# Kernel tuning notes

Measured on AMD Instinct MI355X. Metric: run time of the kernel, lower is better.

## Reference

```python
import jax, jax.numpy as jnp
import numpy as np

N, T, D_FEAT, H = 8192, 60, 6, 64
NEG_SLOPE = 0.01  # torch LeakyReLU default


def setup_inputs() -> dict:
    key = jax.random.key(0)
    ks = jax.random.split(key, 20)
    s = lambda k, shape, fan: jax.random.normal(k, shape, jnp.float32) * (1.0 / np.sqrt(fan))
    inp = {
        'x': jax.random.normal(ks[0], (N, T, D_FEAT), jnp.float32),
        # LSTM layer 0 (input D_FEAT) and layer 1 (input H); gate order i,f,g,o
        'Wih0': s(ks[1], (4 * H, D_FEAT), H), 'Whh0': s(ks[2], (4 * H, H), H),
        'bih0': s(ks[3], (4 * H,), H), 'bhh0': s(ks[4], (4 * H,), H),
        'Wih1': s(ks[5], (4 * H, H), H), 'Whh1': s(ks[6], (4 * H, H), H),
        'bih1': s(ks[7], (4 * H,), H), 'bhh1': s(ks[8], (4 * H,), H),
        # GAT layer: transformation Linear(H,H) and attention vector a [2H,1] (randn in torch)
        'Wt': s(ks[9], (H, H), H), 'bt': s(ks[10], (H,), H),
        'a': jax.random.normal(ks[11], (2 * H, 1), jnp.float32),
        # fc and fc_out
        'Wfc': s(ks[12], (H, H), H), 'bfc': s(ks[13], (H,), H),
        'Wout': s(ks[14], (1, H), H), 'bout': s(ks[15], (1,), H),
    }
    return inp


def _lstm_layer(x, Wih, Whh, bih, bhh):
    # x: [N, T, Din] -> outputs [N, T, H]
    xg = jnp.einsum('ntd,gd->ntg', x, Wih) + bih + bhh  # precompute input gates

    def step(carry, xt):
        h, c = carry
        gates = xt + h @ Whh.T  # [N, 4H]
        i, f, g, o = jnp.split(gates, 4, axis=-1)
        c = jax.nn.sigmoid(f) * c + jax.nn.sigmoid(i) * jnp.tanh(g)
        h = jax.nn.sigmoid(o) * jnp.tanh(c)
        return (h, c), h

    n = x.shape[0]
    h0 = jnp.zeros((n, Whh.shape[1]), x.dtype)
    (_, _), hs = jax.lax.scan(step, (h0, h0), jnp.swapaxes(xg, 0, 1))
    return jnp.swapaxes(hs, 0, 1)


def _gat_layer(x, Wt, bt, a):
    # att[i,j] = leaky_relu(a1 . Wx_j + a2 . Wx_i); softmax over j; out = att @ x
    h = x @ Wt.T + bt                    # [N, H]
    hdim = h.shape[1]
    s1 = (h @ a[:hdim]).squeeze(-1)      # a1 . Wx_j  -> column term
    s2 = (h @ a[hdim:]).squeeze(-1)      # a2 . Wx_i  -> row term
    scores = jax.nn.leaky_relu(s2[:, None] + s1[None, :], NEG_SLOPE)  # [N, N]
    att = jax.nn.softmax(scores, axis=1)
    return att @ x


def reference(x, Wih0, Whh0, bih0, bhh0, Wih1, Whh1, bih1, bhh1,
              Wt, bt, a, Wfc, bfc, Wout, bout):
    out = _lstm_layer(x, Wih0, Whh0, bih0, bhh0)
    out = _lstm_layer(out, Wih1, Whh1, bih1, bhh1)
    last = out[:, -1, :]                 # [N, H]
    hidden = _gat_layer(last, Wt, bt, a) + last  # num_layers_gat = 1
    hidden = jax.nn.leaky_relu(hidden @ Wfc.T + bfc, NEG_SLOPE)
    return (hidden @ Wout.T + bout).squeeze(-1)  # [N]
```

## Files before the change

### kernel.cpp

```cpp
#include <hip/hip_runtime.h>

#define NN 8192
#define TT 60
#define DF 6
#define HH 64
#define GG 256
#define RS 132
#define CH 32
#define NB 256

typedef _Float16 half8 __attribute__((ext_vector_type(8)));
typedef float f32x4 __attribute__((ext_vector_type(4)));
#define MFMA16(a, b, c) __builtin_amdgcn_mfma_f32_16x16x32_f16((a), (b), (c), 0, 0, 0)

#define LOG2E 1.44269504f

__device__ __forceinline__ float lrelu_(float x) { return x > 0.0f ? x : 0.01f * x; }

__device__ __forceinline__ float lstm_act2(float gi, float gf, float gg, float go,
                                           float& c)
{
    const float ei = __builtin_amdgcn_exp2f(gi * -LOG2E);
    const float ef = __builtin_amdgcn_exp2f(gf * -LOG2E);
    const float eg = __builtin_amdgcn_exp2f(fminf(gg * (-2.f * LOG2E), 63.f));
    const float sf = __builtin_amdgcn_rcpf(1.f + ef);
    const float tg_si = (1.f - eg) * __builtin_amdgcn_rcpf((1.f + ei) * (1.f + eg));
    c = __builtin_fmaf(sf, c, tg_si);
    const float eo = __builtin_amdgcn_exp2f(go * -LOG2E);
    const float ec = __builtin_amdgcn_exp2f(fminf(c * (-2.f * LOG2E), 63.f));
    return (1.f - ec) * __builtin_amdgcn_rcpf((1.f + eo) * (1.f + ec));
}

__device__ __forceinline__ half8 ldw8(const float* __restrict__ p) {
    const float4* q = (const float4*)p;
    float4 u = q[0], v = q[1];
    half8 r;
    r[0]=(_Float16)u.x; r[1]=(_Float16)u.y; r[2]=(_Float16)u.z; r[3]=(_Float16)u.w;
    r[4]=(_Float16)v.x; r[5]=(_Float16)v.y; r[6]=(_Float16)v.z; r[7]=(_Float16)v.w;
    return r;
}

#define SXW (TT * 8 + 8)

__global__ __launch_bounds__(512, 4)
void lstm_fused_kernel(const float* __restrict__ x,
                       const float* __restrict__ Wih0, const float* __restrict__ Whh0,
                       const float* __restrict__ bih0, const float* __restrict__ bhh0,
                       const float* __restrict__ Wih1, const float* __restrict__ Whh1,
                       const float* __restrict__ bih1, const float* __restrict__ bhh1,
                       const float* __restrict__ Wt, const float* __restrict__ bt,
                       const float* __restrict__ av,
                       float* __restrict__ last_out,
                       float* __restrict__ s1g, float* __restrict__ s2g)
{
    __shared__ _Float16 sxp[16][SXW];
    __shared__ _Float16 h0buf[2][16][72];
    __shared__ _Float16 h1buf[2][16][72];
    __shared__ _Float16 zero16[8];
    __shared__ float sv1[HH], sv2[HH], sc12[2];

    const int tid  = threadIdx.x;
    const int w    = tid >> 6;
    const int grp  = w >> 2;
    const int cg   = w & 3;
    const int lane = tid & 63;
    const int quad = lane >> 4;
    const int l15  = lane & 15;
    const int hc   = cg * 16 + l15;
    const int n0   = blockIdx.x * 16;

    for (int i = tid; i < 16 * SXW / 2; i += 512) ((unsigned*)sxp)[i] = 0u;
    for (int i = tid; i < 2 * 16 * 72 / 2; i += 512) ((unsigned*)h0buf)[i] = 0u;
    for (int i = tid; i < 2 * 16 * 72 / 2; i += 512) ((unsigned*)h1buf)[i] = 0u;
    if (tid < 4) ((unsigned*)zero16)[tid] = 0u;
    __syncthreads();

    for (int idx = tid; idx < 16 * TT * DF; idx += 512) {
        const int m = idx / (TT * DF);
        const int r = idx - m * (TT * DF);
        const int t = r / DF;
        const int d = r - t * DF;
        sxp[m][t * 8 + d] = (_Float16)x[(size_t)(n0 + m) * (TT * DF) + r];
    }

    if (tid < HH) {
        float a1 = 0.f, a2 = 0.f;
        #pragma unroll 8
        for (int h = 0; h < HH; h++) {
            const float wt = Wt[h * HH + tid];
            a1 += wt * av[h];
            a2 += wt * av[HH + h];
        }
        sv1[tid] = a1; sv2[tid] = a2;
    } else if (tid == 64 || tid == 65) {
        const float* ap = av + (tid - 64) * HH;
        float c = 0.f;
        #pragma unroll 8
        for (int h = 0; h < HH; h++) c += bt[h] * ap[h];
        sc12[tid - 64] = c;
    }

    half8 wA[4][2], wB[4][2];
    float bias[4];
    half8 hzero;
    #pragma unroll
    for (int j = 0; j < 8; j++) hzero[j] = (_Float16)0.f;

    if (grp == 0) {
        #pragma unroll
        for (int nt = 0; nt < 4; nt++) {
            const int g = nt * 64 + hc;
            wA[nt][0] = ldw8(Whh0 + (size_t)g * HH + quad * 8);
            wA[nt][1] = ldw8(Whh0 + (size_t)g * HH + 32 + quad * 8);
            bias[nt]  = bih0[g] + bhh0[g];
            half8 t = hzero;
            if (quad == 0) {
                #pragma unroll
                for (int j = 0; j < DF; j++) t[j] = (_Float16)Wih0[g * DF + j];
            }
            wB[nt][0] = t;
            wB[nt][1] = hzero;
        }
    } else {
        #pragma unroll
        for (int nt = 0; nt < 4; nt++) {
            const int g = nt * 64 + hc;
            wA[nt][0] = ldw8(Wih1 + (size_t)g * HH + quad * 8);
            wA[nt][1] = ldw8(Wih1 + (size_t)g * HH + 32 + quad * 8);
            wB[nt][0] = ldw8(Whh1 + (size_t)g * HH + quad * 8);
            wB[nt][1] = ldw8(Whh1 + (size_t)g * HH + 32 + quad * 8);
            bias[nt]  = bih1[g] + bhh1[g];
        }
    }

    float cs[4] = {0.f, 0.f, 0.f, 0.f};
    __syncthreads();

    for (int i = 0; i <= TT; i++) {
        const int p = i & 1;
        if (grp == 0) {
            if (i < TT) {
                const half8 a0 = *(const half8*)&h0buf[p][l15][quad * 8];
                const half8 a1 = *(const half8*)&h0buf[p][l15][32 + quad * 8];
                const _Float16* xap = (quad == 0) ? &sxp[l15][i * 8] : zero16;
                const half8 ax = *(const half8*)xap;
                f32x4 gv[4];
                #pragma unroll
                for (int nt = 0; nt < 4; nt++) {
                    f32x4 c; c[0] = bias[nt]; c[1] = bias[nt]; c[2] = bias[nt]; c[3] = bias[nt];
                    c = MFMA16(ax, wB[nt][0], c);
                    c = MFMA16(a0, wA[nt][0], c);
                    c = MFMA16(a1, wA[nt][1], c);
                    gv[nt] = c;
                }
                _Float16 (*h0w)[72] = h0buf[p ^ 1];
                #pragma unroll
                for (int reg = 0; reg < 4; reg++) {
                    const float hv = lstm_act2(gv[0][reg], gv[1][reg], gv[2][reg], gv[3][reg], cs[reg]);
                    h0w[quad * 4 + reg][hc] = (_Float16)hv;
                }
            }
        } else {
            if (i > 0) {
                const half8 a00 = *(const half8*)&h0buf[p][l15][quad * 8];
                const half8 a01 = *(const half8*)&h0buf[p][l15][32 + quad * 8];
                const half8 a10 = *(const half8*)&h1buf[p][l15][quad * 8];
                const half8 a11 = *(const half8*)&h1buf[p][l15][32 + quad * 8];
                f32x4 gv[4];
                #pragma unroll
                for (int nt = 0; nt < 4; nt++) {
                    f32x4 c; c[0] = bias[nt]; c[1] = bias[nt]; c[2] = bias[nt]; c[3] = bias[nt];
                    c = MFMA16(a00, wA[nt][0], c);
                    c = MFMA16(a01, wA[nt][1], c);
                    c = MFMA16(a10, wB[nt][0], c);
                    c = MFMA16(a11, wB[nt][1], c);
                    gv[nt] = c;
                }
                _Float16 (*h1w)[72] = h1buf[p ^ 1];
                #pragma unroll
                for (int reg = 0; reg < 4; reg++) {
                    const float hv = lstm_act2(gv[0][reg], gv[1][reg], gv[2][reg], gv[3][reg], cs[reg]);
                    h1w[quad * 4 + reg][hc] = (_Float16)hv;
                    if (i == TT) last_out[(size_t)(n0 + quad * 4 + reg) * HH + hc] = hv;
                }
            }
        }
        __syncthreads();
    }

    {
        const _Float16 (*hf)[72] = h1buf[1];
        const int r  = tid >> 5;
        const int c0 = tid & 31;
        const float h1a = (float)hf[r][c0];
        const float h1b = (float)hf[r][c0 + 32];
        float p1 = h1a * sv1[c0] + h1b * sv1[c0 + 32];
        float p2 = h1a * sv2[c0] + h1b * sv2[c0 + 32];
        #pragma unroll
        for (int off = 16; off > 0; off >>= 1) {
            p1 += __shfl_xor(p1, off);
            p2 += __shfl_xor(p2, off);
        }
        if (c0 == 0) {
            s1g[n0 + r] = p1 + sc12[0];
            s2g[n0 + r] = p2 + sc12[1];
        }
    }
}

__global__ __launch_bounds__(1024)
void rankfac_kernel(const float* __restrict__ s1g, const float* __restrict__ s2g,
                    float* __restrict__ Z, float* __restrict__ Ai, float* __restrict__ Bi,
                    float* __restrict__ U, float* __restrict__ W,
                    int* __restrict__ iperm, float* __restrict__ sortedD)
{
    __shared__ float sb[NN];
    __shared__ float sredw[16];
    __shared__ int   sRank[32];
    const int tid  = threadIdx.x;
    const int lane = tid & 63;
    const int wv   = tid >> 6;
    const int b    = blockIdx.x;
    const int j0   = b * 32;

    for (int idx = tid; idx < NN; idx += 1024) sb[idx] = s1g[idx];
    if (tid < 32) sRank[tid] = 0;
    __syncthreads();

    float m = -1e30f;
    for (int idx = tid; idx < NN; idx += 1024) m = fmaxf(m, sb[idx]);
    #pragma unroll
    for (int off = 32; off > 0; off >>= 1) m = fmaxf(m, __shfl_xor(m, off));
    if (lane == 0) sredw[wv] = m;
    __syncthreads();
    if (tid == 0) {
        float mm = sredw[0];
        #pragma unroll
        for (int q = 1; q < 16; q++) mm = fmaxf(mm, sredw[q]);
        sredw[0] = mm;
    }
    __syncthreads();
    const float s1max = sredw[0];

    if (tid < 32) {
        const int j = j0 + tid;
        const float z  = s2g[j] + s1max;
        const float mi = lrelu_(z);
        Z[j]  = z;
        Ai[j] = __expf(z - mi);
        Bi[j] = __expf(0.01f * z - mi);
        const float d = sb[j] - s1max;
        U[j] = __expf(d);
        W[j] = __expf(0.01f * d);
    }
    {
        const int jl = tid & 31;
        const int part = tid >> 5;
        const float sj = sb[j0 + jl];
        const int jg = j0 + jl;
        const int k0 = part * (NN / 32);
        const float4* sb4 = (const float4*)&sb[k0];
        int cnt = 0;
        #pragma unroll 8
        for (int it = 0; it < NN / 32 / 4; it++) {
            const float4 v = sb4[it];
            const int kb = k0 + it * 4;
            cnt += (v.x < sj || (v.x == sj && kb + 0 < jg)) ? 1 : 0;
            cnt += (v.y < sj || (v.y == sj && kb + 1 < jg)) ? 1 : 0;
            cnt += (v.z < sj || (v.z == sj && kb + 2 < jg)) ? 1 : 0;
            cnt += (v.w < sj || (v.w == sj && kb + 3 < jg)) ? 1 : 0;
        }
        atomicAdd(&sRank[jl], cnt);
    }
    __syncthreads();
    if (tid < 32) {
        const int r = sRank[tid];
        iperm[r] = j0 + tid;
        sortedD[r] = sb[j0 + tid] - s1max;
    }
}

__global__ __launch_bounds__(256)
void scanA_kernel(const float* __restrict__ last, const float* __restrict__ U,
                  const float* __restrict__ W, const int* __restrict__ iperm,
                  float* __restrict__ chunkSum)
{
    __shared__ int   sj[CH];
    __shared__ float su[CH], sw[CH];
    __shared__ float al[CH][HH], bl[CH][HH];
    const int tid = threadIdx.x;
    const int b   = blockIdx.x;
    if (tid < CH) {
        const int j = iperm[b * CH + tid];
        sj[tid] = j; su[tid] = U[j]; sw[tid] = W[j];
    }
    __syncthreads();
    for (int idx = tid; idx < CH * HH; idx += 256) {
        const int rr = idx >> 6, c = idx & 63;
        const float lv = last[(size_t)sj[rr] * HH + c];
        al[rr][c] = su[rr] * lv;
        bl[rr][c] = sw[rr] * lv;
    }
    __syncthreads();
    if (tid < 130) {
        const int c = tid;
        float s = 0.f;
        if (c < 64) {
            for (int rr = 0; rr < CH; rr++) s += al[rr][c];
        } else if (c < 128) {
            for (int rr = 0; rr < CH; rr++) s += bl[rr][c - 64];
        } else if (c == 128) {
            for (int rr = 0; rr < CH; rr++) s += su[rr];
        } else {
            for (int rr = 0; rr < CH; rr++) s += sw[rr];
        }
        chunkSum[b * RS + c] = s;
    }
}

__global__ __launch_bounds__(256)
void scanC_kernel(const float* __restrict__ last, const float* __restrict__ U,
                  const float* __restrict__ W, const int* __restrict__ iperm,
                  const float* __restrict__ chunkSum, float* __restrict__ PP)
{
    __shared__ int   sj[CH];
    __shared__ float su[CH], sw[CH];
    __shared__ float al[CH][HH], bl[CH][HH];
    const int tid = threadIdx.x;
    const int b   = blockIdx.x;
    if (tid < CH) {
        const int j = iperm[b * CH + tid];
        sj[tid] = j; su[tid] = U[j]; sw[tid] = W[j];
    }
    __syncthreads();
    for (int idx = tid; idx < CH * HH; idx += 256) {
        const int rr = idx >> 6, c = idx & 63;
        const float lv = last[(size_t)sj[rr] * HH + c];
        al[rr][c] = su[rr] * lv;
        bl[rr][c] = sw[rr] * lv;
    }
    __syncthreads();
    if (tid < 130) {
        const int c = tid;
        const bool rev = (c < 64) || (c == 128);
        float run = 0.f;
        if (rev) {
            #pragma unroll 8
            for (int k = 0; k < NB; k++)
                run += (k > b) ? chunkSum[k * RS + c] : 0.f;
            if (b == NB - 1) PP[(size_t)NN * RS + c] = 0.f;
            for (int rr = CH - 1; rr >= 0; rr--) {
                const float val = (c < 64) ? al[rr][c] : su[rr];
                run += val;
                PP[(size_t)(b * CH + rr) * RS + c] = run;
            }
        } else {
            #pragma unroll 8
            for (int k = 0; k < NB; k++)
                run += (k < b) ? chunkSum[k * RS + c] : 0.f;
            for (int rr = 0; rr < CH; rr++) {
                PP[(size_t)(b * CH + rr) * RS + c] = run;
                run += (c < 128) ? bl[rr][c - 64] : sw[rr];
            }
            if (b == NB - 1) PP[(size_t)NN * RS + c] = run;
        }
    }
}

__global__ __launch_bounds__(512)
void applyfc_kernel(const float* __restrict__ last,
                    const float* __restrict__ Z, const float* __restrict__ Ai, const float* __restrict__ Bi,
                    const float* __restrict__ sortedD, const float* __restrict__ PP,
                    const float* __restrict__ Wfc, const float* __restrict__ bfc,
                    const float* __restrict__ Wout, const float* __restrict__ bout,
                    float* __restrict__ out)
{
    __shared__ float sdD[NN];
    __shared__ float sW[HH][HH + 1];
    __shared__ float sbF[HH], saF[HH];
    const int tid = threadIdx.x;
    for (int idx = tid; idx < NN; idx += 512) sdD[idx] = sortedD[idx];
    for (int idx = tid; idx < HH * HH; idx += 512) {
        const int h = idx >> 6, d = idx & 63;
        sW[d][h] = Wfc[idx];
    }
    if (tid < HH) { sbF[tid] = bfc[tid]; saF[tid] = Wout[tid]; }
    __syncthreads();

    const int wv = tid >> 6, lane = tid & 63;
    const int i0 = blockIdx.x * 32 + wv * 4;
    float zi[4]; int lo[4], hi[4];
    #pragma unroll
    for (int q = 0; q < 4; q++) { zi[q] = Z[i0 + q]; lo[q] = 0; hi[q] = NN; }
    for (int iter = 0; iter < 13; iter++) {
        #pragma unroll
        for (int q = 0; q < 4; q++) {
            if (lo[q] < hi[q]) {
                const int mid = (lo[q] + hi[q]) >> 1;
                const float dm = sdD[mid];
                if (zi[q] + dm > 0.f) hi[q] = mid; else lo[q] = mid + 1;
            }
        }
    }
    float gv[4];
    #pragma unroll
    for (int q = 0; q < 4; q++) {
        const int i = i0 + q;
        const float* rowp = PP + (size_t)lo[q] * RS;
        const float pu  = rowp[lane];
        const float pw  = rowp[64 + lane];
        const float pud = rowp[128];
        const float pwd = rowp[129];
        const float ai = Ai[i], bi = Bi[i];
        const float numer = bi * pw + ai * pu;
        const float den   = bi * pwd + ai * pud;
        const float lv = last[(size_t)i * HH + lane];
        gv[q] = numer * __builtin_amdgcn_rcpf(den) + lv;
    }
    const float bo = bout[0];
    #pragma unroll
    for (int q = 0; q < 4; q++) {
        float acc = sbF[lane];
        #pragma unroll
        for (int d = 0; d < HH; d++) acc += __shfl(gv[q], d) * sW[d][lane];
        float prod = lrelu_(acc) * saF[lane];
        #pragma unroll
        for (int off = 32; off > 0; off >>= 1) prod += __shfl_xor(prod, off);
        if (lane == 0) out[i0 + q] = prod + bo;
    }
}

extern "C" void kernel_launch(void* const* d_in, const int* in_sizes, int n_in,
                              void* d_out, int out_size, void* d_ws, size_t ws_size,
                              hipStream_t stream)
{
    (void)in_sizes; (void)n_in; (void)out_size; (void)ws_size;
    const float* x    = (const float*)d_in[0];
    const float* Wih0 = (const float*)d_in[1];
    const float* Whh0 = (const float*)d_in[2];
    const float* bih0 = (const float*)d_in[3];
    const float* bhh0 = (const float*)d_in[4];
    const float* Wih1 = (const float*)d_in[5];
    const float* Whh1 = (const float*)d_in[6];
    const float* bih1 = (const float*)d_in[7];
    const float* bhh1 = (const float*)d_in[8];
    const float* Wt   = (const float*)d_in[9];
    const float* bt   = (const float*)d_in[10];
    const float* a    = (const float*)d_in[11];
    const float* Wfc  = (const float*)d_in[12];
    const float* bfc  = (const float*)d_in[13];
    const float* Wout = (const float*)d_in[14];
    const float* bout = (const float*)d_in[15];
    float* out = (float*)d_out;

    float* ws       = (float*)d_ws;
    float* last     = ws;
    float* s1g      = last + (size_t)NN*HH;
    float* s2g      = s1g + NN;
    float* Z        = s2g + NN;
    float* Ai       = Z + NN;
    float* Bi       = Ai + NN;
    float* U        = Bi + NN;
    float* W        = U + NN;
    float* sortedD  = W + NN;
    int*   iperm    = (int*)(sortedD + NN);
    float* chunkSum = (float*)(iperm + NN);
    float* chunkOfs = chunkSum + NB*RS;
    float* PP       = chunkOfs + NB*RS;

    lstm_fused_kernel<<<dim3(NN / 16), dim3(512), 0, stream>>>(
        x, Wih0, Whh0, bih0, bhh0, Wih1, Whh1, bih1, bhh1,
        Wt, bt, a, last, s1g, s2g);
    rankfac_kernel<<<dim3(NB), dim3(1024), 0, stream>>>(
        s1g, s2g, Z, Ai, Bi, U, W, iperm, sortedD);
    scanA_kernel<<<dim3(NB), dim3(256), 0, stream>>>(last, U, W, iperm, chunkSum);
    scanC_kernel<<<dim3(NB), dim3(256), 0, stream>>>(last, U, W, iperm, chunkSum, PP);
    applyfc_kernel<<<dim3(NB), dim3(512), 0, stream>>>(
        last, Z, Ai, Bi, sortedD, PP, Wfc, bfc, Wout, bout, out);
}
```

Before: 243.5 us.

## Merge post-LSTM kernels into one persistent kernel with grid barriers

Fuses the rank/factor, two scan passes and the apply/fc stage into a single 256-block kernel that uses atomic-counter grid barriers in place of kernel launch boundaries. The barrier counters are reset by the LSTM kernel. The shared al/bl tiles are reused between the two scan phases, so the second gather of last is gone. This is meant to remove three launch gaps and one redundant gather. In exchange it depends on all 256 1024-thread blocks being co-resident (deadlock risk otherwise), leaves the apply stage with half the rows per wave, and uses a spin-wait barrier.

```diff
diff --git a/kernel.cpp b/kernel.cpp
--- a/kernel.cpp
+++ b/kernel.cpp
@@ -40,6 +40,18 @@
     return r;
 }
 
+__device__ __forceinline__ void gridbar(int* cnt, int tid)
+{
+    __syncthreads();
+    if (tid == 0) {
+        __threadfence();
+        __hip_atomic_fetch_add(cnt, 1, __ATOMIC_ACQ_REL, __HIP_MEMORY_SCOPE_AGENT);
+        while (__hip_atomic_load(cnt, __ATOMIC_RELAXED, __HIP_MEMORY_SCOPE_AGENT) < NB) {}
+        __threadfence();
+    }
+    __syncthreads();
+}
+
 #define SXW (TT * 8 + 8)
 
 __global__ __launch_bounds__(512, 4)
@@ -51,7 +63,8 @@
                        const float* __restrict__ Wt, const float* __restrict__ bt,
                        const float* __restrict__ av,
                        float* __restrict__ last_out,
-                       float* __restrict__ s1g, float* __restrict__ s2g)
+                       float* __restrict__ s1g, float* __restrict__ s2g,
+                       int* __restrict__ barp)
 {
     __shared__ _Float16 sxp[16][SXW];
     __shared__ _Float16 h0buf[2][16][72];
@@ -68,6 +81,8 @@
     const int l15  = lane & 15;
     const int hc   = cg * 16 + l15;
     const int n0   = blockIdx.x * 16;
+
+    if (blockIdx.x == 0 && tid < 3) barp[tid] = 0;
 
     for (int i = tid; i < 16 * SXW / 2; i += 512) ((unsigned*)sxp)[i] = 0u;
     for (int i = tid; i < 2 * 16 * 72 / 2; i += 512) ((unsigned*)h0buf)[i] = 0u;
@@ -209,14 +224,25 @@
 }
 
 __global__ __launch_bounds__(1024)
-void rankfac_kernel(const float* __restrict__ s1g, const float* __restrict__ s2g,
-                    float* __restrict__ Z, float* __restrict__ Ai, float* __restrict__ Bi,
-                    float* __restrict__ U, float* __restrict__ W,
-                    int* __restrict__ iperm, float* __restrict__ sortedD)
+void post_kernel(const float* __restrict__ last,
+                 const float* __restrict__ s1g, const float* __restrict__ s2g,
+                 float* __restrict__ Z, float* __restrict__ Ai, float* __restrict__ Bi,
+                 float* __restrict__ U, float* __restrict__ W,
+                 int* __restrict__ iperm, float* __restrict__ sortedD,
+                 float* __restrict__ chunkSum, float* __restrict__ PP,
+                 const float* __restrict__ Wfc, const float* __restrict__ bfc,
+                 const float* __restrict__ Wout, const float* __restrict__ bout,
+                 float* __restrict__ out, int* __restrict__ barp)
 {
     __shared__ float sb[NN];
     __shared__ float sredw[16];
     __shared__ int   sRank[32];
+    __shared__ int   sj[CH];
+    __shared__ float su[CH], sw[CH];
+    __shared__ float al[CH][HH], bl[CH][HH];
+    __shared__ float sW[HH][HH + 1];
+    __shared__ float sbF[HH], saF[HH];
+
     const int tid  = threadIdx.x;
     const int lane = tid & 63;
     const int wv   = tid >> 6;
@@ -256,7 +282,7 @@
     {
         const int jl = tid & 31;
         const int part = tid >> 5;
-        const float sj = sb[j0 + jl];
+        const float sjv = sb[j0 + jl];
         const int jg = j0 + jl;
         const int k0 = part * (NN / 32);
         const float4* sb4 = (const float4*)&sb[k0];
@@ -265,10 +291,10 @@
         for (int it = 0; it < NN / 32 / 4; it++) {
             const float4 v = sb4[it];
             const int kb = k0 + it * 4;
-            cnt += (v.x < sj || (v.x == sj && kb + 0 < jg)) ? 1 : 0;
-            cnt += (v.y < sj || (v.y == sj && kb + 1 < jg)) ? 1 : 0;
-            cnt += (v.z < sj || (v.z == sj && kb + 2 < jg)) ? 1 : 0;
-            cnt += (v.w < sj || (v.w == sj && kb + 3 < jg)) ? 1 : 0;
+            cnt += (v.x < sjv || (v.x == sjv && kb + 0 < jg)) ? 1 : 0;
+            cnt += (v.y < sjv || (v.y == sjv && kb + 1 < jg)) ? 1 : 0;
+            cnt += (v.z < sjv || (v.z == sjv && kb + 2 < jg)) ? 1 : 0;
+            cnt += (v.w < sjv || (v.w == sjv && kb + 3 < jg)) ? 1 : 0;
         }
         atomicAdd(&sRank[jl], cnt);
     }
@@ -278,24 +304,15 @@
         iperm[r] = j0 + tid;
         sortedD[r] = sb[j0 + tid] - s1max;
     }
-}
-
-__global__ __launch_bounds__(256)
-void scanA_kernel(const float* __restrict__ last, const float* __restrict__ U,
-                  const float* __restrict__ W, const int* __restrict__ iperm,
-                  float* __restrict__ chunkSum)
-{
-    __shared__ int   sj[CH];
-    __shared__ float su[CH], sw[CH];
-    __shared__ float al[CH][HH], bl[CH][HH];
-    const int tid = threadIdx.x;
-    const int b   = blockIdx.x;
+
+    gridbar(barp + 0, tid);
+
     if (tid < CH) {
         const int j = iperm[b * CH + tid];
         sj[tid] = j; su[tid] = U[j]; sw[tid] = W[j];
     }
     __syncthreads();
-    for (int idx = tid; idx < CH * HH; idx += 256) {
+    for (int idx = tid; idx < CH * HH; idx += 1024) {
         const int rr = idx >> 6, c = idx & 63;
         const float lv = last[(size_t)sj[rr] * HH + c];
         al[rr][c] = su[rr] * lv;
@@ -316,30 +333,9 @@
         }
         chunkSum[b * RS + c] = s;
     }
-}
-
-__global__ __launch_bounds__(256)
-void scanC_kernel(const float* __restrict__ last, const float* __restrict__ U,
-                  const float* __restrict__ W, const int* __restrict__ iperm,
-                  const float* __restrict__ chunkSum, float* __restrict__ PP)
-{
-    __shared__ int   sj[CH];
-    __shared__ float su[CH], sw[CH];
-    __shared__ float al[CH][HH], bl[CH][HH];
-    const int tid = threadIdx.x;
-    const int b   = blockIdx.x;
-    if (tid < CH) {
-        const int j = iperm[b * CH + tid];
-        sj[tid] = j; su[tid] = U[j]; sw[tid] = W[j];
-    }
-    __syncthreads();
-    for (int idx = tid; idx < CH * HH; idx += 256) {
-        const int rr = idx >> 6, c = idx & 63;
-        const float lv = last[(size_t)sj[rr] * HH + c];
-        al[rr][c] = su[rr] * lv;
-        bl[rr][c] = sw[rr] * lv;
-    }
-    __syncthreads();
+
+    gridbar(barp + 1, tid);
+
     if (tid < 130) {
         const int c = tid;
         const bool rev = (c < 64) || (c == 128);
@@ -365,46 +361,34 @@
             if (b == NB - 1) PP[(size_t)NN * RS + c] = run;
         }
     }
-}
-
-__global__ __launch_bounds__(512)
-void applyfc_kernel(const float* __restrict__ last,
-                    const float* __restrict__ Z, const float* __restrict__ Ai, const float* __restrict__ Bi,
-                    const float* __restrict__ sortedD, const float* __restrict__ PP,
-                    const float* __restrict__ Wfc, const float* __restrict__ bfc,
-                    const float* __restrict__ Wout, const float* __restrict__ bout,
-                    float* __restrict__ out)
-{
-    __shared__ float sdD[NN];
-    __shared__ float sW[HH][HH + 1];
-    __shared__ float sbF[HH], saF[HH];
-    const int tid = threadIdx.x;
-    for (int idx = tid; idx < NN; idx += 512) sdD[idx] = sortedD[idx];
-    for (int idx = tid; idx < HH * HH; idx += 512) {
+
+    gridbar(barp + 2, tid);
+
+    for (int idx = tid; idx < NN; idx += 1024) sb[idx] = sortedD[idx];
+    for (int idx = tid; idx < HH * HH; idx += 1024) {
         const int h = idx >> 6, d = idx & 63;
         sW[d][h] = Wfc[idx];
     }
     if (tid < HH) { sbF[tid] = bfc[tid]; saF[tid] = Wout[tid]; }
     __syncthreads();
 
-    const int wv = tid >> 6, lane = tid & 63;
-    const int i0 = blockIdx.x * 32 + wv * 4;
-    float zi[4]; int lo[4], hi[4];
+    const int i0 = b * 32 + wv * 2;
+    float zi[2]; int lo[2], hi[2];
     #pragma unroll
-    for (int q = 0; q < 4; q++) { zi[q] = Z[i0 + q]; lo[q] = 0; hi[q] = NN; }
+    for (int q = 0; q < 2; q++) { zi[q] = Z[i0 + q]; lo[q] = 0; hi[q] = NN; }
     for (int iter = 0; iter < 13; iter++) {
         #pragma unroll
-        for (int q = 0; q < 4; q++) {
+        for (int q = 0; q < 2; q++) {
             if (lo[q] < hi[q]) {
                 const int mid = (lo[q] + hi[q]) >> 1;
-                const float dm = sdD[mid];
+                const float dm = sb[mid];
                 if (zi[q] + dm > 0.f) hi[q] = mid; else lo[q] = mid + 1;
             }
         }
     }
-    float gv[4];
+    float gv[2];
     #pragma unroll
-    for (int q = 0; q < 4; q++) {
+    for (int q = 0; q < 2; q++) {
         const int i = i0 + q;
         const float* rowp = PP + (size_t)lo[q] * RS;
         const float pu  = rowp[lane];
@@ -419,7 +403,7 @@
     }
     const float bo = bout[0];
     #pragma unroll
-    for (int q = 0; q < 4; q++) {
+    for (int q = 0; q < 2; q++) {
         float acc = sbF[lane];
         #pragma unroll
         for (int d = 0; d < HH; d++) acc += __shfl(gv[q], d) * sW[d][lane];
@@ -467,14 +451,12 @@
     float* chunkSum = (float*)(iperm + NN);
     float* chunkOfs = chunkSum + NB*RS;
     float* PP       = chunkOfs + NB*RS;
+    int*   barp     = (int*)(PP + (size_t)(NN + 1) * RS);
 
     lstm_fused_kernel<<<dim3(NN / 16), dim3(512), 0, stream>>>(
         x, Wih0, Whh0, bih0, bhh0, Wih1, Whh1, bih1, bhh1,
-        Wt, bt, a, last, s1g, s2g);
-    rankfac_kernel<<<dim3(NB), dim3(1024), 0, stream>>>(
-        s1g, s2g, Z, Ai, Bi, U, W, iperm, sortedD);
-    scanA_kernel<<<dim3(NB), dim3(256), 0, stream>>>(last, U, W, iperm, chunkSum);
-    scanC_kernel<<<dim3(NB), dim3(256), 0, stream>>>(last, U, W, iperm, chunkSum, PP);
-    applyfc_kernel<<<dim3(NB), dim3(512), 0, stream>>>(
-        last, Z, Ai, Bi, sortedD, PP, Wfc, bfc, Wout, bout, out);
-}
+        Wt, bt, a, last, s1g, s2g, barp);
+    post_kernel<<<dim3(NB), dim3(1024), 0, stream>>>(
+        last, s1g, s2g, Z, Ai, Bi, U, W, iperm, sortedD, chunkSum, PP,
+        Wfc, bfc, Wout, bout, out, barp);
+}
```

New measurement: 291.6 us. 19.8% more time.
